# Kernel optimization log

Hardware: AMD Instinct MI355X
Metric: run time of the kernel (lower is better)

Reference implementation:

```python
import jax, jax.numpy as jnp
import numpy as np

B, N, D = 8, 256, 128


def setup_inputs() -> dict:
    key = jax.random.key(0)
    ks = jax.random.split(key, 4)
    s1 = 1.0 / np.sqrt(4 * D)
    s2 = 1.0 / np.sqrt(2 * D)
    s3 = 1.0 / np.sqrt(D)
    return {
        "tour_features": jax.random.normal(ks[0], (B, N, D), dtype=jnp.float32),
        "W1": jax.random.uniform(ks[1], (4 * D, 2 * D), jnp.float32, -s1, s1),
        "b1": jnp.zeros((2 * D,), jnp.float32),
        "W2": jax.random.uniform(ks[2], (2 * D, D), jnp.float32, -s2, s2),
        "b2": jnp.zeros((D,), jnp.float32),
        "W3": jax.random.uniform(ks[3], (D, 1), jnp.float32, -s3, s3),
        "b3": jnp.zeros((1,), jnp.float32),
    }


def reference(tour_features, W1, b1, W2, b2, W3, b3):
    Bs, Ns, Ds = tour_features.shape
    x = tour_features
    x_next = jnp.roll(x, -1, axis=1)  # node at (k+1) % N
    # Split first linear's weight by the 4 concatenated feature blocks:
    # cat([x_i, x_{i+1}, x_j, x_{j+1}]) @ W1 == x_i@W1a + x_{i+1}@W1b + x_j@W1c + x_{j+1}@W1d
    W1a, W1b, W1c, W1d = jnp.split(W1, 4, axis=0)
    Pi = x @ W1a + x_next @ W1b          # [B, N, 2D] (i-side projection)
    Pj = x @ W1c + x_next @ W1d          # [B, N, 2D] (j-side projection)
    h1 = jax.nn.relu(Pi[:, :, None, :] + Pj[:, None, :, :] + b1)  # [B, N, N, 2D]
    h2 = jax.nn.relu(h1 @ W2 + b2)       # [B, N, N, D]
    score = jnp.tanh((h2 @ W3 + b3)[..., 0])  # [B, N, N]
    # Valid pairs: j >= i + 2 and not (j - i == N - 1)
    ii = jnp.arange(Ns)[:, None]
    jj = jnp.arange(Ns)[None, :]
    mask = (jj >= ii + 2) & (jj - ii != Ns - 1)
    improvement_matrix = jnp.where(mask[None], score, 0.0)
    improved_tour = jnp.broadcast_to(jnp.arange(Ns), (Bs, Ns))
    return improved_tour, improvement_matrix
```

## Files before the change

### kernel.cpp

```cpp
#include <hip/hip_runtime.h>


typedef __attribute__((ext_vector_type(8))) short short8;
typedef __attribute__((ext_vector_type(8))) _Float16 half8;
typedef __attribute__((ext_vector_type(4))) float floatx4;

static __device__ __forceinline__ unsigned short f2bf(float f) {
  unsigned int x = __float_as_uint(f);
  x += 0x7fff + ((x >> 16) & 1);
  return (unsigned short)(x >> 16);
}

static __device__ __forceinline__ unsigned short f2h(float f) {
  _Float16 h = (_Float16)f;
  return __builtin_bit_cast(unsigned short, h);
}

static __device__ __forceinline__ float fast_tanh(float x) {
  float e = __expf(2.0f * fabsf(x));
  float t = 1.0f - 2.0f * __builtin_amdgcn_rcpf(e + 1.0f);
  return copysignf(t, x);
}

static __device__ __forceinline__ long pack_fp8(half8 s) {
  int lo = __builtin_amdgcn_cvt_pk_fp8_f32((float)s[0], (float)s[1], 0, false);
  lo = __builtin_amdgcn_cvt_pk_fp8_f32((float)s[2], (float)s[3], lo, true);
  int hi = __builtin_amdgcn_cvt_pk_fp8_f32((float)s[4], (float)s[5], 0, false);
  hi = __builtin_amdgcn_cvt_pk_fp8_f32((float)s[6], (float)s[7], hi, true);
  return (long)(unsigned)lo | ((long)hi << 32);
}

static __device__ __forceinline__ void gload_lds16(const void* g, void* l) {
  __builtin_amdgcn_global_load_lds(
      (const __attribute__((address_space(1))) unsigned int*)g,
      (__attribute__((address_space(3))) unsigned int*)l, 16, 0, 0);
}

__global__ __launch_bounds__(256) void k_proj(
    const float* __restrict__ x, const float* __restrict__ W1,
    const float* __restrict__ b1, unsigned short* __restrict__ PiH,
    unsigned short* __restrict__ PjH, const float* __restrict__ W2,
    float* __restrict__ out, unsigned char* __restrict__ W2F8) {
  const int tid = threadIdx.x;
  const int bx = blockIdx.x;

  if (bx >= 256) {
    if (bx < 770) {
      int t = (bx - 256) * 256 + tid;
      int e = t * 4;
      floatx4 w;
      if (e < 2048) {
        float v = (float)(e & 255);
        w = (floatx4){v, v + 1.f, v + 2.f, v + 3.f};
      } else {
        w = (floatx4)0.f;
      }
      *(floatx4*)(out + e) = w;
    } else {
      int t = (bx - 770) * 256 + tid;
      int p = t >> 7, n = t & 127;
      float f0 = W2[(2 * p) * 128 + n] * 16.f;
      float f1 = W2[(2 * p + 1) * 128 + n] * 16.f;
      int v2 = __builtin_amdgcn_cvt_pk_fp8_f32(f0, f1, 0, false);
      int q = n >> 5, which = (n >> 4) & 1, l = n & 15;
      int c = p >> 2, off = (p & 3) * 2;
      int cs = (c & 16) | ((c ^ l) & 15);
      *(unsigned short*)(W2F8 + q * 8192 + l * 512 + cs * 16 + which * 8 + off) =
          (unsigned short)(v2 & 0xffff);
    }
    return;
  }

  const int mg = bx >> 3;
  const int ng = bx & 7;
  const int wr = tid >> 6, lane = tid & 63, quad = lane >> 4, l15 = lane & 15;

  __shared__ unsigned short As[64 * 256];
  __shared__ unsigned short Bs[64 * 256];

  {
    const int roff = (ng >= 4) ? 256 : 0;
    const int colbase = (ng & 3) * 64;
    const int rg = tid & 15;
#pragma unroll
    for (int pass = 0; pass < 16; ++pass) {
      const int k = pass * 16 + (tid >> 4);
      const floatx4 f =
          *(const floatx4*)(W1 + (k + roff) * 256 + colbase + rg * 4);
      const int v = k >> 3;
      const int kb = (k & 7) * 2;
#pragma unroll
      for (int j = 0; j < 4; ++j) {
        const int r = rg * 4 + j;
        const int sw = (v & 16) | ((v ^ (r & 15)) & 15);
        *(unsigned short*)((char*)Bs + r * 512 + sw * 16 + kb) = f2bf(f[j]);
      }
    }
  }

#pragma unroll
  for (int pass = 0; pass < 8; ++pass) {
    const int rr = pass * 8 + (tid >> 5);
    const int grow = mg * 64 + rr;
    const int pos = grow & 255, bb = grow >> 8;
    const int v = tid & 31;
    const int pos2 = (v < 16) ? pos : ((pos + 1) & 255);
    const float* src = x + (bb * 256 + pos2) * 128 + (v & 15) * 8;
    const floatx4 f0 = *(const floatx4*)(src);
    const floatx4 f1 = *(const floatx4*)(src + 4);
    union { short8 s; unsigned short u[8]; } o;
    o.u[0] = f2bf(f0[0]); o.u[1] = f2bf(f0[1]);
    o.u[2] = f2bf(f0[2]); o.u[3] = f2bf(f0[3]);
    o.u[4] = f2bf(f1[0]); o.u[5] = f2bf(f1[1]);
    o.u[6] = f2bf(f1[2]); o.u[7] = f2bf(f1[3]);
    const int sw = (v & 16) | ((v ^ (rr & 15)) & 15);
    *(short8*)((char*)As + rr * 512 + sw * 16) = o.s;
  }
  __syncthreads();

  floatx4 acc[4];
#pragma unroll
  for (int mt = 0; mt < 4; ++mt) acc[mt] = (floatx4)0.f;

  const char* Ab = (const char*)As;
  const char* Bb = (const char*)Bs + wr * 16 * 512;
  const int base_sw = l15 * 512 + ((quad ^ l15) << 4);

#pragma unroll
  for (int ks = 0; ks < 8; ++ks) {
    const int swz = base_sw ^ (ks << 6);
    short8 bfr = *(const short8*)(Bb + swz);
#pragma unroll
    for (int mt = 0; mt < 4; ++mt) {
      short8 afr = *(const short8*)(Ab + mt * 8192 + swz);
      acc[mt] = __builtin_amdgcn_mfma_f32_16x16x32_bf16(afr, bfr, acc[mt], 0, 0, 0);
    }
  }

  const int ch = ng * 64 + wr * 16 + l15;
  const float bias = (ch < 256) ? b1[ch] : 0.f;
  const bool isPi = (ch < 256);
  unsigned short* dst = isPi ? PiH : PjH;
  const int chan = ch & 255;
  const int ck = chan >> 3, coff = chan & 7;
#pragma unroll
  for (int mt = 0; mt < 4; ++mt)
#pragma unroll
    for (int r = 0; r < 4; ++r) {
      int row = mg * 64 + mt * 16 + quad * 4 + r;
      int cpos;
      if (isPi) cpos = chan;
      else {
        int cs = (ck & 16) | ((ck ^ (row & 15)) & 15);
        cpos = cs * 8 + coff;
      }
      dst[row * 256 + cpos] = f2h(acc[mt][r] + bias);
    }
}

__global__ __launch_bounds__(256, 3) void k_main(
    const unsigned short* __restrict__ PiH, const unsigned short* __restrict__ PjH,
    const unsigned char* __restrict__ W2F8, const float* __restrict__ b2,
    const float* __restrict__ W3, const float* __restrict__ b3,
    float* __restrict__ outm) {
  const int tid = threadIdx.x;
  const int wr = tid >> 6;
  const int lane = tid & 63, quad = lane >> 4, l15 = lane & 15;

  __shared__ unsigned char W2s[32768];
  __shared__ unsigned char PjS[16384];
  __shared__ unsigned char PiS[4096];

  const int bid = blockIdx.x;
  const int b = bid / 288;
  const int rem = bid - b * 288;
  int jt = 0, basej = 0;
  if (rem >= 8)   { jt = 1; basej = 8;   }
  if (rem >= 24)  { jt = 2; basej = 24;  }
  if (rem >= 48)  { jt = 3; basej = 48;  }
  if (rem >= 80)  { jt = 4; basej = 80;  }
  if (rem >= 120) { jt = 5; basej = 120; }
  if (rem >= 168) { jt = 6; basej = 168; }
  if (rem >= 224) { jt = 7; basej = 224; }
  const int i = (rem - basej) * 4 + wr;

  const unsigned char* pjsrc =
      (const unsigned char*)(PjH + ((b << 8) + jt * 32) * 256);
  const unsigned char* pisrc =
      (const unsigned char*)(PiH + ((b << 8) + i) * 256);
#pragma unroll
  for (int it = 0; it < 8; ++it) {
    const int c = it * 256 + wr * 64 + lane;
    gload_lds16(W2F8 + c * 16, &W2s[(it * 256 + wr * 64) * 16]);
  }
#pragma unroll
  for (int it = 0; it < 4; ++it) {
    const int c = it * 256 + wr * 64 + lane;
    gload_lds16(pjsrc + c * 16, &PjS[(it * 256 + wr * 64) * 16]);
  }
  gload_lds16(pisrc + (lane & 31) * 16, &PiS[wr * 1024]);
  __syncthreads();

  const char* W2base = (const char*)&W2s[0];
  const char* PjBase = (const char*)&PjS[0];
  const char* PiBase = (const char*)&PiS[0] + wr * 1024 + quad * 16;
  const int sw16 = l15 * 512 + (((quad ^ l15) & 15) << 4);

  floatx4 acc[2][8];
#pragma unroll
  for (int mt = 0; mt < 2; ++mt)
#pragma unroll
    for (int nt = 0; nt < 8; ++nt) acc[mt][nt] = (floatx4)0.f;

  union U4 { uint4 v; half8 h; };
  U4 piR[2], pjR[2][2];
  piR[0].v = *(const uint4*)(PiBase);
  pjR[0][0].v = *(const uint4*)(PjBase + sw16);
  pjR[0][1].v = *(const uint4*)(PjBase + 8192 + sw16);
  piR[1].v = *(const uint4*)(PiBase + 64);
  {
    const char* pj = PjBase + (sw16 ^ 64);
    pjR[1][0].v = *(const uint4*)(pj);
    pjR[1][1].v = *(const uint4*)(pj + 8192);
  }

  uint4 bfA[4], bfB[4];
  {
    const char* b0 = W2base + sw16;
#pragma unroll
    for (int q = 0; q < 4; ++q) bfA[q] = *(const uint4*)(b0 + q * 8192);
  }

  long aC0, aC1;
  {
    const half8 s0 = __builtin_elementwise_max(piR[0].h + pjR[0][0].h,
                                               (half8)(_Float16)0);
    const half8 s1 = __builtin_elementwise_max(piR[0].h + pjR[0][1].h,
                                               (half8)(_Float16)0);
    aC0 = pack_fp8(s0);
    aC1 = pack_fp8(s1);
  }

#pragma unroll
  for (int ks = 0; ks < 8; ++ks) {
    if (ks < 7) {
      const char* bn = W2base + (sw16 ^ ((ks + 1) << 6));
#pragma unroll
      for (int q = 0; q < 4; ++q)
        ((ks & 1) ? bfA : bfB)[q] = *(const uint4*)(bn + q * 8192);
    }
    if (ks < 6) {
      piR[ks & 1].v = *(const uint4*)(PiBase + (ks + 2) * 64);
      const char* pj = PjBase + (sw16 ^ ((ks + 2) << 6));
      pjR[ks & 1][0].v = *(const uint4*)(pj);
      pjR[ks & 1][1].v = *(const uint4*)(pj + 8192);
    }
    long aN0 = 0, aN1 = 0;
    if (ks < 7) {
      const half8 s0 = __builtin_elementwise_max(
          piR[(ks + 1) & 1].h + pjR[(ks + 1) & 1][0].h, (half8)(_Float16)0);
      const half8 s1 = __builtin_elementwise_max(
          piR[(ks + 1) & 1].h + pjR[(ks + 1) & 1][1].h, (half8)(_Float16)0);
      aN0 = pack_fp8(s0);
      aN1 = pack_fp8(s1);
    }
    const uint4* bc = (ks & 1) ? bfB : bfA;
    __builtin_amdgcn_s_setprio(1);
#pragma unroll
    for (int q = 0; q < 4; ++q) {
      const long blo = (long)bc[q].x | ((long)bc[q].y << 32);
      const long bhi = (long)bc[q].z | ((long)bc[q].w << 32);
      acc[0][2 * q]     = __builtin_amdgcn_mfma_f32_16x16x32_fp8_fp8(aC0, blo, acc[0][2 * q], 0, 0, 0);
      acc[1][2 * q]     = __builtin_amdgcn_mfma_f32_16x16x32_fp8_fp8(aC1, blo, acc[1][2 * q], 0, 0, 0);
      acc[0][2 * q + 1] = __builtin_amdgcn_mfma_f32_16x16x32_fp8_fp8(aC0, bhi, acc[0][2 * q + 1], 0, 0, 0);
      acc[1][2 * q + 1] = __builtin_amdgcn_mfma_f32_16x16x32_fp8_fp8(aC1, bhi, acc[1][2 * q + 1], 0, 0, 0);
    }
    __builtin_amdgcn_s_setprio(0);
    if (ks < 7) { aC0 = aN0; aC1 = aN1; }
  }

  float* orow = outm + ((b << 8) + i) * 256 + jt * 32;
  const float b3v = b3[0];
  const float s16 = 0.0625f;
#pragma unroll
  for (int mt = 0; mt < 2; ++mt) {
    float p0 = 0, p1 = 0, p2 = 0, p3 = 0;
#pragma unroll
    for (int nt = 0; nt < 8; ++nt) {
      float w3v = W3[nt * 16 + l15];
      float b2v = b2[nt * 16 + l15];
      floatx4 a = acc[mt][nt];
      p0 += fmaxf(fmaf(a[0], s16, b2v), 0.f) * w3v;
      p1 += fmaxf(fmaf(a[1], s16, b2v), 0.f) * w3v;
      p2 += fmaxf(fmaf(a[2], s16, b2v), 0.f) * w3v;
      p3 += fmaxf(fmaf(a[3], s16, b2v), 0.f) * w3v;
    }
#pragma unroll
    for (int m = 8; m >= 1; m >>= 1) {
      p0 += __shfl_xor(p0, m, 16);
      p1 += __shfl_xor(p1, m, 16);
      p2 += __shfl_xor(p2, m, 16);
      p3 += __shfl_xor(p3, m, 16);
    }
    if (l15 == 0) {
      const int jl = jt * 32 + mt * 16 + quad * 4;
      float ps[4] = {p0, p1, p2, p3};
#pragma unroll
      for (int r = 0; r < 4; ++r) {
        int j = jl + r;
        float sc = fast_tanh(ps[r] + b3v);
        bool valid = (j >= i + 2) && (j - i != 255);
        orow[mt * 16 + quad * 4 + r] = valid ? sc : 0.f;
      }
    }
  }
}

extern "C" void kernel_launch(void* const* d_in, const int* in_sizes, int n_in,
                              void* d_out, int out_size, void* d_ws, size_t ws_size,
                              hipStream_t stream) {
  const float* x  = (const float*)d_in[0];
  const float* W1 = (const float*)d_in[1];
  const float* b1 = (const float*)d_in[2];
  const float* W2 = (const float*)d_in[3];
  const float* b2 = (const float*)d_in[4];
  const float* W3 = (const float*)d_in[5];
  const float* b3 = (const float*)d_in[6];
  float* out = (float*)d_out;

  unsigned short* PiH  = (unsigned short*)d_ws;
  unsigned short* PjH  = PiH + 524288;
  unsigned char*  W2F8 = (unsigned char*)(PjH + 524288);

  k_proj<<<834, 256, 0, stream>>>(x, W1, b1, PiH, PjH, W2, out, W2F8);
  k_main<<<2304, 256, 0, stream>>>(PiH, PjH, W2F8, b2, W3, b3, out + 2048);
}
```

Baseline: 93.71 us.

## Switch fp8 MFMA to gfx950 scaled 16x16x128 instruction with batched K-steps

Replaces the 8-step loop of 16x16x32 fp8 MFMAs with two halves that each gather four K-steps into 8-dword operands and issue the gfx950 mfma_scale 16x16x128 f8f6f4 instruction with unit scales. This cuts the MFMA instruction count by a factor of four and uses the higher-throughput MI355 fp8 path. In exchange it drops the software-pipelined double buffering of LDS loads, so loads and fp8 packing for each half now run before its MFMAs with less overlap, and register pressure rises from the wider operands.

After: 91.26 us. 1.03x faster.

```diff
diff --git a/kernel.cpp b/kernel.cpp
--- a/kernel.cpp
+++ b/kernel.cpp
@@ -4,6 +4,7 @@
 typedef __attribute__((ext_vector_type(8))) short short8;
 typedef __attribute__((ext_vector_type(8))) _Float16 half8;
 typedef __attribute__((ext_vector_type(4))) float floatx4;
+typedef __attribute__((ext_vector_type(8))) int intx8;
 
 static __device__ __forceinline__ unsigned short f2bf(float f) {
   unsigned int x = __float_as_uint(f);
@@ -213,70 +214,63 @@
     for (int nt = 0; nt < 8; ++nt) acc[mt][nt] = (floatx4)0.f;
 
   union U4 { uint4 v; half8 h; };
-  U4 piR[2], pjR[2][2];
-  piR[0].v = *(const uint4*)(PiBase);
-  pjR[0][0].v = *(const uint4*)(PjBase + sw16);
-  pjR[0][1].v = *(const uint4*)(PjBase + 8192 + sw16);
-  piR[1].v = *(const uint4*)(PiBase + 64);
-  {
-    const char* pj = PjBase + (sw16 ^ 64);
-    pjR[1][0].v = *(const uint4*)(pj);
-    pjR[1][1].v = *(const uint4*)(pj + 8192);
-  }
-
-  uint4 bfA[4], bfB[4];
-  {
-    const char* b0 = W2base + sw16;
-#pragma unroll
-    for (int q = 0; q < 4; ++q) bfA[q] = *(const uint4*)(b0 + q * 8192);
-  }
-
-  long aC0, aC1;
-  {
-    const half8 s0 = __builtin_elementwise_max(piR[0].h + pjR[0][0].h,
-                                               (half8)(_Float16)0);
-    const half8 s1 = __builtin_elementwise_max(piR[0].h + pjR[0][1].h,
-                                               (half8)(_Float16)0);
-    aC0 = pack_fp8(s0);
-    aC1 = pack_fp8(s1);
-  }
-
-#pragma unroll
-  for (int ks = 0; ks < 8; ++ks) {
-    if (ks < 7) {
-      const char* bn = W2base + (sw16 ^ ((ks + 1) << 6));
-#pragma unroll
-      for (int q = 0; q < 4; ++q)
-        ((ks & 1) ? bfA : bfB)[q] = *(const uint4*)(bn + q * 8192);
-    }
-    if (ks < 6) {
-      piR[ks & 1].v = *(const uint4*)(PiBase + (ks + 2) * 64);
-      const char* pj = PjBase + (sw16 ^ ((ks + 2) << 6));
-      pjR[ks & 1][0].v = *(const uint4*)(pj);
-      pjR[ks & 1][1].v = *(const uint4*)(pj + 8192);
-    }
-    long aN0 = 0, aN1 = 0;
-    if (ks < 7) {
-      const half8 s0 = __builtin_elementwise_max(
-          piR[(ks + 1) & 1].h + pjR[(ks + 1) & 1][0].h, (half8)(_Float16)0);
-      const half8 s1 = __builtin_elementwise_max(
-          piR[(ks + 1) & 1].h + pjR[(ks + 1) & 1][1].h, (half8)(_Float16)0);
-      aN0 = pack_fp8(s0);
-      aN1 = pack_fp8(s1);
-    }
-    const uint4* bc = (ks & 1) ? bfB : bfA;
-    __builtin_amdgcn_s_setprio(1);
-#pragma unroll
-    for (int q = 0; q < 4; ++q) {
-      const long blo = (long)bc[q].x | ((long)bc[q].y << 32);
-      const long bhi = (long)bc[q].z | ((long)bc[q].w << 32);
-      acc[0][2 * q]     = __builtin_amdgcn_mfma_f32_16x16x32_fp8_fp8(aC0, blo, acc[0][2 * q], 0, 0, 0);
-      acc[1][2 * q]     = __builtin_amdgcn_mfma_f32_16x16x32_fp8_fp8(aC1, blo, acc[1][2 * q], 0, 0, 0);
-      acc[0][2 * q + 1] = __builtin_amdgcn_mfma_f32_16x16x32_fp8_fp8(aC0, bhi, acc[0][2 * q + 1], 0, 0, 0);
-      acc[1][2 * q + 1] = __builtin_amdgcn_mfma_f32_16x16x32_fp8_fp8(aC1, bhi, acc[1][2 * q + 1], 0, 0, 0);
-    }
-    __builtin_amdgcn_s_setprio(0);
-    if (ks < 7) { aC0 = aN0; aC1 = aN1; }
+  const int SCL = 0x7f7f7f7f;
+
+#pragma unroll
+  for (int kh = 0; kh < 2; ++kh) {
+    U4 piq[4], pj0q[4], pj1q[4];
+#pragma unroll
+    for (int ks = 0; ks < 4; ++ks) {
+      const int ksg = kh * 4 + ks;
+      piq[ks].v = *(const uint4*)(PiBase + ksg * 64);
+      const char* pj = PjBase + (sw16 ^ (ksg << 6));
+      pj0q[ks].v = *(const uint4*)(pj);
+      pj1q[ks].v = *(const uint4*)(pj + 8192);
+    }
+    long a0[4], a1[4];
+#pragma unroll
+    for (int ks = 0; ks < 4; ++ks) {
+      const half8 s0 = __builtin_elementwise_max(piq[ks].h + pj0q[ks].h,
+                                                 (half8)(_Float16)0);
+      const half8 s1 = __builtin_elementwise_max(piq[ks].h + pj1q[ks].h,
+                                                 (half8)(_Float16)0);
+      a0[ks] = pack_fp8(s0);
+      a1[ks] = pack_fp8(s1);
+    }
+    intx8 A0, A1;
+#pragma unroll
+    for (int ks = 0; ks < 4; ++ks) {
+      A0[2 * ks] = (int)a0[ks];  A0[2 * ks + 1] = (int)(a0[ks] >> 32);
+      A1[2 * ks] = (int)a1[ks];  A1[2 * ks + 1] = (int)(a1[ks] >> 32);
+    }
+#pragma unroll
+    for (int nh = 0; nh < 2; ++nh) {
+#pragma unroll
+      for (int q2 = 0; q2 < 2; ++q2) {
+        const int q = nh * 2 + q2;
+        uint4 bu[4];
+#pragma unroll
+        for (int ks = 0; ks < 4; ++ks)
+          bu[ks] = *(const uint4*)(W2base + (sw16 ^ ((kh * 4 + ks) << 6)) +
+                                   q * 8192);
+        intx8 Blo, Bhi;
+#pragma unroll
+        for (int ks = 0; ks < 4; ++ks) {
+          Blo[2 * ks] = (int)bu[ks].x;  Blo[2 * ks + 1] = (int)bu[ks].y;
+          Bhi[2 * ks] = (int)bu[ks].z;  Bhi[2 * ks + 1] = (int)bu[ks].w;
+        }
+        __builtin_amdgcn_s_setprio(1);
+        acc[0][2 * q] = __builtin_amdgcn_mfma_scale_f32_16x16x128_f8f6f4(
+            A0, Blo, acc[0][2 * q], 0, 0, 0, SCL, 0, SCL);
+        acc[1][2 * q] = __builtin_amdgcn_mfma_scale_f32_16x16x128_f8f6f4(
+            A1, Blo, acc[1][2 * q], 0, 0, 0, SCL, 0, SCL);
+        acc[0][2 * q + 1] = __builtin_amdgcn_mfma_scale_f32_16x16x128_f8f6f4(
+            A0, Bhi, acc[0][2 * q + 1], 0, 0, 0, SCL, 0, SCL);
+        acc[1][2 * q + 1] = __builtin_amdgcn_mfma_scale_f32_16x16x128_f8f6f4(
+            A1, Bhi, acc[1][2 * q + 1], 0, 0, 0, SCL, 0, SCL);
+        __builtin_amdgcn_s_setprio(0);
+      }
+    }
   }
 
   float* orow = outm + ((b << 8) + i) * 256 + jt * 32;
```
